# Kernel tuning notes

Hardware: AMD Instinct MI355X
Metric: run time of the kernel (lower is better)

The kernel has to match this reference:

```python
import jax, jax.numpy as jnp
import numpy as np

M_DIM = 32          # vec_dim m
L1 = L2 = L3 = L4 = 3
L_TOT = L1 * L2 * L3 * L4   # 81
R = 2               # rank1..rank4 window size
B_SZ = 4
D_SZ = 16           # D1 = D2 = D3 = D4


def _make_bbasis():
    # Bbasis[idx, i] = prod_k cos(2*pi*(j_k+1)/(i+2)), idx = flattened (j1,j2,j3,j4)
    i = jnp.arange(M_DIM, dtype=jnp.float32)
    def c(Lk):
        j = jnp.arange(Lk, dtype=jnp.float32)
        return jnp.cos(2.0 * jnp.pi * (j[:, None] + 1.0) / (i[None, :] + 2.0))  # [Lk, m]
    c1, c2, c3, c4 = c(L1), c(L2), c(L3), c(L4)
    Bb = (c1[:, None, None, None, :] * c2[None, :, None, None, :]
          * c3[None, None, :, None, :] * c4[None, None, None, :, :])
    return Bb.reshape(L_TOT, M_DIM)


def _window_basis_idx(n1, n2, n3, n4):
    # linear mode, drop: window top-left coords are 0..n_k-1 with step 1
    j1 = jnp.arange(n1) % L1
    j2 = jnp.arange(n2) % L2
    j3 = jnp.arange(n3) % L3
    j4 = jnp.arange(n4) % L4
    idx = (((j1[:, None, None, None] * L2 + j2[None, :, None, None]) * L3
            + j3[None, None, :, None]) * L4 + j4[None, None, None, :])
    return idx.reshape(-1)  # [n_windows]


def setup_inputs() -> dict:
    key = jax.random.key(0)
    k1, k2, k3 = jax.random.split(key, 3)
    arr_batch = jax.random.normal(k1, (B_SZ, D_SZ, D_SZ, D_SZ, D_SZ, M_DIM), dtype=jnp.float32)
    # M initialized near identity (nn.init.eye_ + perturbation so grads are non-trivial)
    M = jnp.eye(M_DIM, dtype=jnp.float32) + 0.01 * jax.random.normal(k2, (M_DIM, M_DIM), dtype=jnp.float32)
    # Acoeff ~ U(-0.1, 0.1) as in reset_parameters
    Acoeff = jax.random.uniform(k3, (M_DIM, L_TOT), dtype=jnp.float32, minval=-0.1, maxval=0.1)
    Bbasis = _make_bbasis()  # fixed buffer, computed deterministically
    return {"arr_batch": arr_batch, "M": M, "Acoeff": Acoeff, "Bbasis": Bbasis}


def reference(arr_batch, M, Acoeff, Bbasis):
    Bsz, D1, D2, D3, D4, m = arr_batch.shape
    # map every vector through M (x @ M.T); avg-pooling commutes with the linear map,
    # matching `mapped = windows @ M.T` then mean over the window
    mapped = jnp.einsum('bpqrsm,nm->bpqrsn', arr_batch, M)
    # 4D sliding window (rank=2 per dim, stride 1, 'drop' -> VALID), rank_op='avg'
    win = (1, R, R, R, R, 1)
    agg = jax.lax.reduce_window(mapped, 0.0, jax.lax.add, win, (1,) * 6, 'VALID') / float(R ** 4)
    n1, n2, n3, n4 = agg.shape[1:5]
    n_win = n1 * n2 * n3 * n4
    agg = agg.reshape(Bsz, n_win, m)            # [B, W, m]
    idx = _window_basis_idx(n1, n2, n3, n4)     # [W]
    phi = Bbasis[idx]                           # [W, m]
    # t_k = Acoeff[:, j_k] * (Bbasis[j_k, :] . agg_k); representation = mean_k t_k
    s = jnp.einsum('bwm,wm->bw', agg, phi)      # [B, W]
    t = s[:, :, None] * Acoeff.T[idx][None]     # [B, W, m]
    return t.mean(axis=1)                       # [B, m]
```

## Files before the change

### kernel.cpp

```cpp
#include <hip/hip_runtime.h>


static __device__ __forceinline__ void add4(float4& a, const float4& b) {
    a.x += b.x; a.y += b.y; a.z += b.z; a.w += b.w;
}
static __device__ __forceinline__ void fma4(float4& a, float w, const float4& b) {
    a.x = fmaf(w, b.x, a.x); a.y = fmaf(w, b.y, a.y);
    a.z = fmaf(w, b.z, a.z); a.w = fmaf(w, b.w, a.w);
}

__global__ __launch_bounds__(128) void sdd4_v(
    const float* __restrict__ arr,
    float* __restrict__ V,
    float* __restrict__ out)
{
    __shared__ float4 U_lds[400];

    const int t  = threadIdx.x;
    const int bx = blockIdx.x;
    const int b  = bx >> 8;
    const int p  = (bx >> 4) & 15;
    const int q  = bx & 15;

    if (bx == 0) out[t] = 0.f;

    const int r  = t >> 3;
    const int mv = t & 7;
    const float4* A4 = reinterpret_cast<const float4*>(arr);
    const size_t tile = (size_t)((b * 16 + p) * 16 + q) * 2048;

    float4 u0 = make_float4(0.f, 0.f, 0.f, 0.f), u1 = u0, u2 = u0;
    #pragma unroll
    for (int s = 0; s < 16; ++s) {
        float4 x = A4[tile + (size_t)(r * 16 + s) * 8 + mv];
        if ((0x36DBu >> s) & 1) add4(u0, x);
        if ((0x6DB6u >> s) & 1) add4(u1, x);
        if ((0xDB6Cu >> s) & 1) add4(u2, x);
    }
    U_lds[r * 25 +      mv] = u0;
    U_lds[r * 25 +  8 + mv] = u1;
    U_lds[r * 25 + 16 + mv] = u2;
    __syncthreads();

    if (t < 72) {
        const int j3  = t / 24;
        const int rem = t % 24;
        const int j4  = rem >> 3;
        const int mv2 = rem & 7;
        const unsigned msk = (j3 == 0) ? 0x36DBu : (j3 == 1 ? 0x6DB6u : 0xDB6Cu);
        float4 acc = make_float4(0.f, 0.f, 0.f, 0.f);
        #pragma unroll
        for (int rr = 0; rr < 16; ++rr) {
            float w = (float)((msk >> rr) & 1u);
            fma4(acc, w, U_lds[rr * 25 + j4 * 8 + mv2]);
        }
        const int jj = j3 * 3 + j4;
        float4* V4 = reinterpret_cast<float4*>(V);
        V4[((b * 9 + jj) * 256 + p * 16 + q) * 8 + mv2] = acc;
    }
}

__global__ __launch_bounds__(256) void sdd4_reduce(
    const float* __restrict__ V,
    const float* __restrict__ Mmat,
    const float* __restrict__ Bbasis,
    const float* __restrict__ Acoeff,
    float* __restrict__ out)
{
    __shared__ float M_lds[32 * 33];
    __shared__ float Bb_lds[9 * 33];
    __shared__ float Vp[8 * 9 * 33];
    __shared__ float Vs[9 * 33];
    __shared__ float Y_lds[9 * 33];
    __shared__ float Sf[9];

    const int t   = threadIdx.x;
    const int blk = blockIdx.x;
    const int b   = blk / 9;
    const int jj  = blk % 9;

    const float4* M4 = reinterpret_cast<const float4*>(Mmat);
    if (t < 256) {
        float4 v = M4[t];
        float* dst = &M_lds[(t >> 3) * 33 + (t & 7) * 4];
        dst[0] = v.x; dst[1] = v.y; dst[2] = v.z; dst[3] = v.w;
    }
    const float4* B4 = reinterpret_cast<const float4*>(Bbasis);
    if (t < 72) {
        const int k = t >> 3, f4 = t & 7;
        float4 v = B4[(k * 9 + jj) * 8 + f4];
        float* dst = &Bb_lds[k * 33 + f4 * 4];
        dst[0] = v.x; dst[1] = v.y; dst[2] = v.z; dst[3] = v.w;
    }

    const int g = t >> 5;
    const int m = t & 31;
    const float* Vb = V + (size_t)blk * 8192;
    float acc[9];
    #pragma unroll
    for (int c = 0; c < 9; ++c) acc[c] = 0.f;
    #pragma unroll 4
    for (int u = 0; u < 32; ++u) {
        const int pq = g * 32 + u;
        const int p  = pq >> 4;
        const int q  = pq & 15;
        const float v = Vb[pq * 32 + m];
        const unsigned e1 = ((0x36DBu >> p) & 1u) | (((0x6DB6u >> p) & 1u) << 1)
                          | (((0xDB6Cu >> p) & 1u) << 2);
        const unsigned e2 = ((0x36DBu >> q) & 1u) | (((0x6DB6u >> q) & 1u) << 1)
                          | (((0xDB6Cu >> q) & 1u) << 2);
        #pragma unroll
        for (int c = 0; c < 9; ++c)
            if (((e1 >> (c / 3)) & 1u) && ((e2 >> (c % 3)) & 1u))
                acc[c] += v;
    }
    #pragma unroll
    for (int c = 0; c < 9; ++c) Vp[(g * 9 + c) * 33 + m] = acc[c];
    __syncthreads();

    for (int o = t; o < 288; o += 256) {
        const int c = o >> 5, mm = o & 31;
        float s = 0.f;
        #pragma unroll
        for (int gg = 0; gg < 8; ++gg) s += Vp[(gg * 9 + c) * 33 + mm];
        Vs[c * 33 + mm] = s;
    }
    __syncthreads();

    for (int o = t; o < 288; o += 256) {
        const int c = o >> 5, n = o & 31;
        float s = 0.f;
        #pragma unroll
        for (int mm = 0; mm < 32; ++mm)
            s = fmaf(M_lds[n * 33 + mm], Vs[c * 33 + mm], s);
        Y_lds[c * 33 + n] = s;
    }
    __syncthreads();

    if (t < 9) {
        float s = 0.f;
        #pragma unroll
        for (int n = 0; n < 32; ++n)
            s = fmaf(Bb_lds[t * 33 + n], Y_lds[t * 33 + n], s);
        Sf[t] = s;
    }
    __syncthreads();

    if (t < 32) {
        float z = 0.f;
        #pragma unroll
        for (int c = 0; c < 9; ++c)
            z = fmaf(Acoeff[t * 81 + c * 9 + jj], Sf[c], z);
        atomicAdd(&out[b * 32 + t], z * (1.0f / 810000.0f));
    }
}

extern "C" void kernel_launch(void* const* d_in, const int* in_sizes, int n_in,
                              void* d_out, int out_size, void* d_ws, size_t ws_size,
                              hipStream_t stream) {
    const float* arr    = (const float*)d_in[0];
    const float* Mmat   = (const float*)d_in[1];
    const float* Acoeff = (const float*)d_in[2];
    const float* Bbasis = (const float*)d_in[3];
    float* V = (float*)d_ws;

    sdd4_v     <<<dim3(1024), dim3(128), 0, stream>>>(arr, V, (float*)d_out);
    sdd4_reduce<<<dim3(36),   dim3(256), 0, stream>>>(V, Mmat, Bbasis, Acoeff,
                                                      (float*)d_out);
}
```

Before: 84.48 us.

## Fuse window-sum and reduction kernels into one cooperative launch with grid sync

Merges the two kernels into a single cooperative kernel. The first phase's partial sums go to global memory through relaxed atomic stores, and after a grid-wide barrier 36 blocks perform the reduction with 128 threads each. This is meant to remove the second kernel launch and the inter-kernel gap. The cost is a grid barrier, cooperative-launch overhead, and twice the per-thread work in the reduce phase.

```diff
diff --git a/kernel.cpp b/kernel.cpp
--- a/kernel.cpp
+++ b/kernel.cpp
@@ -1,4 +1,7 @@
 #include <hip/hip_runtime.h>
+#include <hip/hip_cooperative_groups.h>
+
+namespace cg = cooperative_groups;
 
 
 static __device__ __forceinline__ void add4(float4& a, const float4& b) {
@@ -9,12 +12,21 @@
     a.z = fmaf(w, b.z, a.z); a.w = fmaf(w, b.w, a.w);
 }
 
-__global__ __launch_bounds__(128) void sdd4_v(
+__global__ __launch_bounds__(128) void sdd4_all(
     const float* __restrict__ arr,
+    const float* __restrict__ Mmat,
+    const float* __restrict__ Bbasis,
+    const float* __restrict__ Acoeff,
     float* __restrict__ V,
     float* __restrict__ out)
 {
     __shared__ float4 U_lds[400];
+    __shared__ float  M_lds[32 * 33];
+    __shared__ float  Bb_lds[9 * 33];
+    __shared__ float  Vp[4 * 9 * 33];
+    __shared__ float  Vs[9 * 33];
+    __shared__ float  Y_lds[9 * 33];
+    __shared__ float  Sf[9];
 
     const int t  = threadIdx.x;
     const int bx = blockIdx.x;
@@ -22,7 +34,9 @@
     const int p  = (bx >> 4) & 15;
     const int q  = bx & 15;
 
-    if (bx == 0) out[t] = 0.f;
+    if (bx == 0)
+        __hip_atomic_store(&out[t], 0.f, __ATOMIC_RELAXED,
+                           __HIP_MEMORY_SCOPE_AGENT);
 
     const int r  = t >> 3;
     const int mv = t & 7;
@@ -55,103 +69,95 @@
             fma4(acc, w, U_lds[rr * 25 + j4 * 8 + mv2]);
         }
         const int jj = j3 * 3 + j4;
-        float4* V4 = reinterpret_cast<float4*>(V);
-        V4[((b * 9 + jj) * 256 + p * 16 + q) * 8 + mv2] = acc;
-    }
-}
-
-__global__ __launch_bounds__(256) void sdd4_reduce(
-    const float* __restrict__ V,
-    const float* __restrict__ Mmat,
-    const float* __restrict__ Bbasis,
-    const float* __restrict__ Acoeff,
-    float* __restrict__ out)
-{
-    __shared__ float M_lds[32 * 33];
-    __shared__ float Bb_lds[9 * 33];
-    __shared__ float Vp[8 * 9 * 33];
-    __shared__ float Vs[9 * 33];
-    __shared__ float Y_lds[9 * 33];
-    __shared__ float Sf[9];
-
-    const int t   = threadIdx.x;
-    const int blk = blockIdx.x;
-    const int b   = blk / 9;
-    const int jj  = blk % 9;
-
-    const float4* M4 = reinterpret_cast<const float4*>(Mmat);
-    if (t < 256) {
-        float4 v = M4[t];
-        float* dst = &M_lds[(t >> 3) * 33 + (t & 7) * 4];
-        dst[0] = v.x; dst[1] = v.y; dst[2] = v.z; dst[3] = v.w;
-    }
-    const float4* B4 = reinterpret_cast<const float4*>(Bbasis);
-    if (t < 72) {
-        const int k = t >> 3, f4 = t & 7;
-        float4 v = B4[(k * 9 + jj) * 8 + f4];
-        float* dst = &Bb_lds[k * 33 + f4 * 4];
-        dst[0] = v.x; dst[1] = v.y; dst[2] = v.z; dst[3] = v.w;
+        float* dst = &V[(size_t)(((b * 9 + jj) * 256 + p * 16 + q) * 8 + mv2) * 4];
+        __hip_atomic_store(&dst[0], acc.x, __ATOMIC_RELAXED, __HIP_MEMORY_SCOPE_AGENT);
+        __hip_atomic_store(&dst[1], acc.y, __ATOMIC_RELAXED, __HIP_MEMORY_SCOPE_AGENT);
+        __hip_atomic_store(&dst[2], acc.z, __ATOMIC_RELAXED, __HIP_MEMORY_SCOPE_AGENT);
+        __hip_atomic_store(&dst[3], acc.w, __ATOMIC_RELAXED, __HIP_MEMORY_SCOPE_AGENT);
     }
 
-    const int g = t >> 5;
-    const int m = t & 31;
-    const float* Vb = V + (size_t)blk * 8192;
-    float acc[9];
-    #pragma unroll
-    for (int c = 0; c < 9; ++c) acc[c] = 0.f;
-    #pragma unroll 4
-    for (int u = 0; u < 32; ++u) {
-        const int pq = g * 32 + u;
-        const int p  = pq >> 4;
-        const int q  = pq & 15;
-        const float v = Vb[pq * 32 + m];
-        const unsigned e1 = ((0x36DBu >> p) & 1u) | (((0x6DB6u >> p) & 1u) << 1)
-                          | (((0xDB6Cu >> p) & 1u) << 2);
-        const unsigned e2 = ((0x36DBu >> q) & 1u) | (((0x6DB6u >> q) & 1u) << 1)
-                          | (((0xDB6Cu >> q) & 1u) << 2);
+    __threadfence();
+    cg::this_grid().sync();
+
+    if (bx < 36) {
+        const int bb = bx / 9;
+        const int jj = bx % 9;
+
+        const float4* M4 = reinterpret_cast<const float4*>(Mmat);
+        for (int i = t; i < 256; i += 128) {
+            float4 v = M4[i];
+            float* dst = &M_lds[(i >> 3) * 33 + (i & 7) * 4];
+            dst[0] = v.x; dst[1] = v.y; dst[2] = v.z; dst[3] = v.w;
+        }
+        const float4* B4 = reinterpret_cast<const float4*>(Bbasis);
+        if (t < 72) {
+            const int k = t >> 3, f4 = t & 7;
+            float4 v = B4[(k * 9 + jj) * 8 + f4];
+            float* dst = &Bb_lds[k * 33 + f4 * 4];
+            dst[0] = v.x; dst[1] = v.y; dst[2] = v.z; dst[3] = v.w;
+        }
+
+        const int g = t >> 5;
+        const int m = t & 31;
+        const float* Vb = V + (size_t)bx * 8192;
+        float acc[9];
         #pragma unroll
-        for (int c = 0; c < 9; ++c)
-            if (((e1 >> (c / 3)) & 1u) && ((e2 >> (c % 3)) & 1u))
-                acc[c] += v;
-    }
-    #pragma unroll
-    for (int c = 0; c < 9; ++c) Vp[(g * 9 + c) * 33 + m] = acc[c];
-    __syncthreads();
+        for (int c = 0; c < 9; ++c) acc[c] = 0.f;
+        #pragma unroll 4
+        for (int u = 0; u < 64; ++u) {
+            const int pq = g * 64 + u;
+            const int pp = pq >> 4;
+            const int qq = pq & 15;
+            const float v = __hip_atomic_load(&Vb[pq * 32 + m], __ATOMIC_RELAXED,
+                                              __HIP_MEMORY_SCOPE_AGENT);
+            const unsigned e1 = ((0x36DBu >> pp) & 1u) | (((0x6DB6u >> pp) & 1u) << 1)
+                              | (((0xDB6Cu >> pp) & 1u) << 2);
+            const unsigned e2 = ((0x36DBu >> qq) & 1u) | (((0x6DB6u >> qq) & 1u) << 1)
+                              | (((0xDB6Cu >> qq) & 1u) << 2);
+            #pragma unroll
+            for (int c = 0; c < 9; ++c)
+                if (((e1 >> (c / 3)) & 1u) && ((e2 >> (c % 3)) & 1u))
+                    acc[c] += v;
+        }
+        #pragma unroll
+        for (int c = 0; c < 9; ++c) Vp[(g * 9 + c) * 33 + m] = acc[c];
+        __syncthreads();
 
-    for (int o = t; o < 288; o += 256) {
-        const int c = o >> 5, mm = o & 31;
-        float s = 0.f;
-        #pragma unroll
-        for (int gg = 0; gg < 8; ++gg) s += Vp[(gg * 9 + c) * 33 + mm];
-        Vs[c * 33 + mm] = s;
-    }
-    __syncthreads();
+        for (int o = t; o < 288; o += 128) {
+            const int c = o >> 5, mm = o & 31;
+            float s = 0.f;
+            #pragma unroll
+            for (int gg = 0; gg < 4; ++gg) s += Vp[(gg * 9 + c) * 33 + mm];
+            Vs[c * 33 + mm] = s;
+        }
+        __syncthreads();
 
-    for (int o = t; o < 288; o += 256) {
-        const int c = o >> 5, n = o & 31;
-        float s = 0.f;
-        #pragma unroll
-        for (int mm = 0; mm < 32; ++mm)
-            s = fmaf(M_lds[n * 33 + mm], Vs[c * 33 + mm], s);
-        Y_lds[c * 33 + n] = s;
-    }
-    __syncthreads();
+        for (int o = t; o < 288; o += 128) {
+            const int c = o >> 5, n = o & 31;
+            float s = 0.f;
+            #pragma unroll
+            for (int mm = 0; mm < 32; ++mm)
+                s = fmaf(M_lds[n * 33 + mm], Vs[c * 33 + mm], s);
+            Y_lds[c * 33 + n] = s;
+        }
+        __syncthreads();
 
-    if (t < 9) {
-        float s = 0.f;
-        #pragma unroll
-        for (int n = 0; n < 32; ++n)
-            s = fmaf(Bb_lds[t * 33 + n], Y_lds[t * 33 + n], s);
-        Sf[t] = s;
-    }
-    __syncthreads();
+        if (t < 9) {
+            float s = 0.f;
+            #pragma unroll
+            for (int n = 0; n < 32; ++n)
+                s = fmaf(Bb_lds[t * 33 + n], Y_lds[t * 33 + n], s);
+            Sf[t] = s;
+        }
+        __syncthreads();
 
-    if (t < 32) {
-        float z = 0.f;
-        #pragma unroll
-        for (int c = 0; c < 9; ++c)
-            z = fmaf(Acoeff[t * 81 + c * 9 + jj], Sf[c], z);
-        atomicAdd(&out[b * 32 + t], z * (1.0f / 810000.0f));
+        if (t < 32) {
+            float z = 0.f;
+            #pragma unroll
+            for (int c = 0; c < 9; ++c)
+                z = fmaf(Acoeff[t * 81 + c * 9 + jj], Sf[c], z);
+            atomicAdd(&out[bb * 32 + t], z * (1.0f / 810000.0f));
+        }
     }
 }
 
@@ -162,9 +168,11 @@
     const float* Mmat   = (const float*)d_in[1];
     const float* Acoeff = (const float*)d_in[2];
     const float* Bbasis = (const float*)d_in[3];
-    float* V = (float*)d_ws;
+    float* V    = (float*)d_ws;
+    float* outp = (float*)d_out;
 
-    sdd4_v     <<<dim3(1024), dim3(128), 0, stream>>>(arr, V, (float*)d_out);
-    sdd4_reduce<<<dim3(36),   dim3(256), 0, stream>>>(V, Mmat, Bbasis, Acoeff,
-                                                      (float*)d_out);
+    void* args[] = {(void*)&arr, (void*)&Mmat, (void*)&Bbasis,
+                    (void*)&Acoeff, (void*)&V, (void*)&outp};
+    hipLaunchCooperativeKernel((void*)sdd4_all, dim3(1024), dim3(128),
+                               args, 0, stream);
 }
```

Measured after the change: 265.6 us. +214.4%, slower.
